# Performance work log

Measured on AMD Instinct MI355X. Metric: run time of the kernel, lower is better.

Reference implementation:

```python
import jax, jax.numpy as jnp
import numpy as np

N, E, M = 100000, 1600000, 10000
D_IN, D_HID, D_OUT = 128, 128, 128


def setup_inputs() -> dict:
    key = jax.random.key(0)
    ks = jax.random.split(key, 16)
    feat = jax.random.normal(ks[0], (N, D_IN), dtype=jnp.float32)
    src = jax.random.randint(ks[1], (E,), 0, N, dtype=jnp.int32)
    dst = jax.random.randint(ks[2], (E,), 0, N, dtype=jnp.int32)
    masked_offset = jax.random.randint(ks[3], (M,), 0, N, dtype=jnp.int32)
    def xavier(k, shape):
        fan_in, fan_out = shape[0], shape[1]
        a = jnp.sqrt(6.0 / (fan_in + fan_out))
        return jax.random.uniform(k, shape, jnp.float32, -a, a)
    return {
        'feat': feat, 'src': src, 'dst': dst, 'masked_offset': masked_offset,
        # GraphConv layers (weight [in,out], bias [out])
        'W1': xavier(ks[4], (D_IN, D_HID)), 'b1': jnp.zeros((D_HID,), jnp.float32),
        'W2': xavier(ks[5], (D_HID, D_HID)), 'b2': jnp.zeros((D_HID,), jnp.float32),
        # fusion MLP
        'Wm1': xavier(ks[6], (D_HID + D_IN, D_HID)), 'bm1': jnp.zeros((D_HID,), jnp.float32),
        'Wm2': xavier(ks[7], (D_HID, D_HID)), 'bm2': jnp.zeros((D_HID,), jnp.float32),
        'Wm3': xavier(ks[8], (D_HID, D_OUT)),  # final Linear has bias=False
    }


def _graph_conv_right(h, src, dst, W, b, inv_deg):
    # DGL GraphConv(norm='right'): aggregate src features at dst, divide by in-degree.
    # Apply weight first (in_feats >= out_feats path) -- mathematically identical.
    hw = h @ W                                   # [N, out]
    agg = jax.ops.segment_sum(hw[src], dst, num_segments=N)  # scatter-add over edges
    return agg * inv_deg + b


def reference(feat, src, dst, masked_offset, W1, b1, W2, b2, Wm1, bm1, Wm2, bm2, Wm3):
    ones = jnp.ones((E,), jnp.float32)
    deg = jax.ops.segment_sum(ones, dst, num_segments=N)
    inv_deg = (1.0 / jnp.clip(deg, 1.0, None))[:, None]      # [N,1]
    # GCN layer 1 + ReLU (Identity norm)
    h = jax.nn.relu(_graph_conv_right(feat, src, dst, W1, b1, inv_deg))
    # GCN layer 2 (last layer: no activation; dropout no-op at eval)
    h = _graph_conv_right(h, src, dst, W2, b2, inv_deg)
    # fusion == 'cat': relu(Identity(h[masked])) concat raw features
    hm = jax.nn.relu(h[masked_offset])                       # [M, H]
    x = jnp.concatenate([hm, feat[masked_offset]], axis=1)   # [M, H+D]
    x = jax.nn.relu(x @ Wm1 + bm1)
    x = jax.nn.relu(x @ Wm2 + bm2)
    return x @ Wm3
```

## Files before the change

kernel.cpp:

```cpp
#include <hip/hip_runtime.h>

#define NN 100000
#define NE 1600000
#define NM 10000
#define NSB 256
#define SUBN 391
#define CAP2 7424
#define PCH 2048

typedef __attribute__((ext_vector_type(8))) short bf16x8;
typedef __attribute__((ext_vector_type(4))) float f32x4;

__device__ inline float4 ld4(const float* p) { return *(const float4*)p; }
__device__ inline float bf2f(unsigned short u) {
  union { unsigned int i; float f; } c; c.i = ((unsigned int)u) << 16; return c.f;
}
__device__ inline unsigned short f2bf(float f) {
  union { float f; unsigned int i; } c; c.f = f;
  unsigned int u = c.i + 0x7fffu + ((c.i >> 16) & 1u);
  return (unsigned short)(u >> 16);
}
__device__ inline void stx(unsigned char* base, int rowBytes, int row, int col,
                           unsigned short val) {
  int bc = col * 2;
  int c = bc >> 4, cp = c ^ (row & 15);
  *(unsigned short*)&base[row * rowBytes + (cp << 4) + (bc & 15)] = val;
}
__device__ inline bf16x8 ldx8(const unsigned char* base, int rowBytes, int row, int kc) {
  return *(const bf16x8*)&base[row * rowBytes + ((kc ^ (row & 15)) << 4)];
}

__global__ __launch_bounds__(256) void part2_k(const int* __restrict__ src,
                                               const int* __restrict__ dst,
                                               unsigned* __restrict__ parts2,
                                               int* __restrict__ pcnt2) {
  __shared__ int cntw[4][NSB];
  __shared__ int basew[4][NSB];
  __shared__ int bstart[NSB + 1];
  __shared__ int gbase[NSB];
  __shared__ int wsum[4];
  __shared__ unsigned buf[PCH];
  __shared__ unsigned char bb[PCH];
  const int tid = threadIdx.x;
  const int wv = tid >> 6;
  const int e0 = blockIdx.x * PCH;

  for (int i = tid; i < 4 * NSB; i += 256) ((int*)cntw)[i] = 0;
  __syncthreads();

  unsigned pk[8];
  int b_[8], lp_[8];
#pragma unroll
  for (int j = 0; j < 8; ++j) {
    int e = e0 + j * 256 + tid;
    bool ok = e < NE;
    int s = ok ? src[e] : 0;
    int d = ok ? dst[e] : 0;
    int b = d / SUBN;
    int ld = d - b * SUBN;
    pk[j] = ((unsigned)ld << 17) | (unsigned)s;
    b_[j] = ok ? b : -1;
    if (ok) lp_[j] = atomicAdd(&cntw[wv][b], 1);
  }
  __syncthreads();
  int t0 = cntw[0][tid], t1 = cntw[1][tid], t2 = cntw[2][tid], t3 = cntw[3][tid];
  int tot = t0 + t1 + t2 + t3;
  int x = tot;
#pragma unroll
  for (int d = 1; d < 64; d <<= 1) {
    int y = __shfl_up(x, d, 64);
    if ((tid & 63) >= d) x += y;
  }
  if ((tid & 63) == 63) wsum[wv] = x;
  __syncthreads();
  int woff = 0;
#pragma unroll
  for (int w = 0; w < 4; ++w) woff += (w < wv) ? wsum[w] : 0;
  int excl = x + woff - tot;
  bstart[tid] = excl;
  basew[0][tid] = excl;
  basew[1][tid] = excl + t0;
  basew[2][tid] = excl + t0 + t1;
  basew[3][tid] = excl + t0 + t1 + t2;
  gbase[tid] = atomicAdd(&pcnt2[tid], tot);
  if (tid == NSB - 1) bstart[NSB] = excl + tot;
  __syncthreads();
#pragma unroll
  for (int j = 0; j < 8; ++j)
    if (b_[j] >= 0) {
      int pos = basew[wv][b_[j]] + lp_[j];
      buf[pos] = pk[j];
      bb[pos] = (unsigned char)b_[j];
    }
  __syncthreads();
  int total = bstart[NSB];
  for (int i = tid; i < total; i += 256) {
    int b = bb[i];
    int gi = gbase[b] + (i - bstart[b]);
    if (gi < CAP2) parts2[(size_t)b * CAP2 + gi] = buf[i];
  }
}

__global__ __launch_bounds__(1024) void deg2_k(const unsigned* __restrict__ parts2,
                                               const int* __restrict__ pcnt2,
                                               int* __restrict__ deg) {
  __shared__ int cnt[SUBN];
  int sb = blockIdx.x;
  int n = min(pcnt2[sb], CAP2);
  const unsigned* p = parts2 + (size_t)sb * CAP2;
  for (int i = threadIdx.x; i < SUBN; i += 1024) cnt[i] = 0;
  __syncthreads();
  for (int i = threadIdx.x; i < n; i += 1024) atomicAdd(&cnt[p[i] >> 17], 1);
  __syncthreads();
  int base = sb * SUBN;
  for (int i = threadIdx.x; i < SUBN; i += 1024)
    if (base + i < NN) deg[base + i] = cnt[i];
}

__global__ __launch_bounds__(1024) void scan1_k(const int* __restrict__ deg,
                                                int* __restrict__ excl,
                                                int* __restrict__ bsum, int n) {
  __shared__ int lds[1024];
  int tid = threadIdx.x;
  int gid = blockIdx.x * 1024 + tid;
  int v = (gid < n) ? deg[gid] : 0;
  lds[tid] = v;
  __syncthreads();
  for (int off = 1; off < 1024; off <<= 1) {
    int t = (tid >= off) ? lds[tid - off] : 0;
    __syncthreads();
    lds[tid] += t;
    __syncthreads();
  }
  if (gid < n) excl[gid] = lds[tid] - v;
  if (tid == 1023) bsum[blockIdx.x] = lds[1023];
}

__global__ void scan2_k(int* __restrict__ bsum, int nb) {
  __shared__ int lds[128];
  int tid = threadIdx.x;
  int v = (tid < nb) ? bsum[tid] : 0;
  lds[tid] = v;
  __syncthreads();
  for (int off = 1; off < 128; off <<= 1) {
    int t = (tid >= off) ? lds[tid - off] : 0;
    __syncthreads();
    lds[tid] += t;
    __syncthreads();
  }
  if (tid < nb) bsum[tid] = lds[tid] - v;
}

__global__ __launch_bounds__(256) void scan3_k(int* __restrict__ excl,
                                               const int* __restrict__ bsum,
                                               const int* __restrict__ deg,
                                               float* __restrict__ inv, int n) {
  int gid = blockIdx.x * 256 + threadIdx.x;
  if (gid < n) {
    excl[gid] += bsum[gid >> 10] + deg[gid];
    inv[gid] = 1.0f / fmaxf((float)deg[gid], 1.0f);
  }
}

__global__ __launch_bounds__(1024) void sort_emit_k(const unsigned* __restrict__ parts2,
                                                    const int* __restrict__ pcnt2,
                                                    const int* __restrict__ offs_end,
                                                    const int* __restrict__ degv,
                                                    int* __restrict__ csr) {
  __shared__ int cur[SUBN];
  __shared__ int sorted[CAP2];
  int sb = blockIdx.x;
  int n = min(pcnt2[sb], CAP2);
  const unsigned* p = parts2 + (size_t)sb * CAP2;
  int base = sb * SUBN;
  int segbase = offs_end[base] - degv[base];
  for (int i = threadIdx.x; i < SUBN; i += 1024) {
    int nd = base + i;
    cur[i] = (nd < NN) ? (offs_end[nd] - degv[nd]) : 0;
  }
  __syncthreads();
  for (int i = threadIdx.x; i < n; i += 1024) {
    unsigned v = p[i];
    int pos = atomicAdd(&cur[v >> 17], 1);
    sorted[pos - segbase] = (int)(v & 0x1FFFFu);
  }
  __syncthreads();
  for (int i = threadIdx.x; i < n; i += 1024) csr[segbase + i] = sorted[i];
}

__global__ __launch_bounds__(256) void tobf_k(const float* __restrict__ x,
                                              unsigned short* __restrict__ y, int n) {
  int idx = (blockIdx.x * 256 + threadIdx.x) * 4;
  if (idx < n) {
    float4 v = ld4(x + idx);
    unsigned int lo = (unsigned int)f2bf(v.x) | ((unsigned int)f2bf(v.y) << 16);
    unsigned int hi = (unsigned int)f2bf(v.z) | ((unsigned int)f2bf(v.w) << 16);
    *(uint2*)(y + idx) = make_uint2(lo, hi);
  }
}

__device__ inline void convfrag(const float* W, unsigned short* Wf, int g) {
  int k8 = (g >> 7) << 3, col = g & 127;
  unsigned short tmp[8];
#pragma unroll
  for (int i = 0; i < 8; ++i) tmp[i] = f2bf(W[(k8 + i) * 128 + col]);
  *(uint4*)&Wf[(size_t)g * 8] = *(const uint4*)tmp;
}
__global__ __launch_bounds__(256) void wconv_k(const float* W1, const float* W2,
                                               const float* Wm1, const float* Wm2,
                                               const float* Wm3,
                                               unsigned short* W1f, unsigned short* W2f,
                                               unsigned short* Wm1f, unsigned short* Wm2f,
                                               unsigned short* Wm3f) {
  int g = blockIdx.x * 256 + threadIdx.x;
  if (g < 2048) convfrag(W1, W1f, g);
  else if (g < 4096) convfrag(W2, W2f, g - 2048);
  else if (g < 8192) convfrag(Wm1, Wm1f, g - 4096);
  else if (g < 10240) convfrag(Wm2, Wm2f, g - 8192);
  else if (g < 12288) convfrag(Wm3, Wm3f, g - 10240);
}

__global__ __launch_bounds__(256) void mark_k(const int* __restrict__ masked,
                                              const int* __restrict__ csr,
                                              const int* __restrict__ offs_end,
                                              const int* __restrict__ degv,
                                              unsigned char* __restrict__ needed) {
  int m = blockIdx.x * 8 + (threadIdx.x >> 5);
  if (m >= NM) return;
  int lane = threadIdx.x & 31;
  int v = masked[m];
  int cnt = degv[v];
  int start = offs_end[v] - cnt;
  for (int i = lane; i < cnt; i += 32) needed[csr[start + i]] = 1;
}

__global__ __launch_bounds__(256) void fused_l1_k(const unsigned short* __restrict__ featbf,
                                                  const int* __restrict__ csr,
                                                  const int* __restrict__ offs_end,
                                                  const int* __restrict__ degv,
                                                  const float* __restrict__ inv,
                                                  const unsigned char* __restrict__ needed,
                                                  const unsigned short* __restrict__ W1f,
                                                  const float* __restrict__ b1,
                                                  unsigned short* __restrict__ h1bf) {
  __shared__ unsigned char lds[64 * 256];
  const int tid = threadIdx.x;
  const int rbase = blockIdx.x * 64;
  {
    int grp = tid >> 5, lane = tid & 31;
    const uint2* fb = (const uint2*)featbf;
    int c = lane >> 1;
    for (int k = 0; k < 8; ++k) {
      int row = grp * 8 + k;
      int v = rbase + row;
      unsigned char* dstp = &lds[row * 256 + (((c ^ (row & 15)) << 4)) + (lane & 1) * 8];
      if (v >= NN || !needed[v]) { *(uint2*)dstp = make_uint2(0u, 0u); continue; }
      int cnt = degv[v];
      int start = offs_end[v] - cnt;
      float a0 = 0.f, a1 = 0.f, a2 = 0.f, a3 = 0.f;
      int nb8 = (cnt + 7) >> 3;
      for (int it = 0; it < nb8; ++it) {
        int b = start + (it << 3);
        int rem = cnt - (it << 3);
        int sidx[8]; float msk[8];
#pragma unroll
        for (int j = 0; j < 8; ++j) {
          bool ok = j < rem;
          sidx[j] = csr[b + (ok ? j : 0)];
          msk[j] = ok ? 1.f : 0.f;
        }
        uint2 x[8];
#pragma unroll
        for (int j = 0; j < 8; ++j) x[j] = fb[(size_t)sidx[j] * 32 + lane];
#pragma unroll
        for (int j = 0; j < 8; ++j) {
          a0 = fmaf(msk[j], bf2f((unsigned short)(x[j].x)), a0);
          a1 = fmaf(msk[j], bf2f((unsigned short)(x[j].x >> 16)), a1);
          a2 = fmaf(msk[j], bf2f((unsigned short)(x[j].y)), a2);
          a3 = fmaf(msk[j], bf2f((unsigned short)(x[j].y >> 16)), a3);
        }
      }
      float iv = inv[v];
      unsigned int lo = (unsigned int)f2bf(a0 * iv) | ((unsigned int)f2bf(a1 * iv) << 16);
      unsigned int hi = (unsigned int)f2bf(a2 * iv) | ((unsigned int)f2bf(a3 * iv) << 16);
      *(uint2*)dstp = make_uint2(lo, hi);
    }
  }
  __syncthreads();
  const int wave = tid >> 6, lane = tid & 63, l15 = lane & 15, l4 = lane >> 4;
  int col0 = wave * 16 + l15, col1 = (wave + 4) * 16 + l15;
  float bias0 = b1[col0], bias1 = b1[col1];
  for (int rsub = 0; rsub < 4; ++rsub) {
    int row = rsub * 16 + l15;
    f32x4 acc0 = {0.f, 0.f, 0.f, 0.f};
    f32x4 acc1 = {0.f, 0.f, 0.f, 0.f};
#pragma unroll
    for (int kt = 0; kt < 4; ++kt) {
      int kc = kt * 4 + l4;
      bf16x8 a = ldx8(lds, 256, row, kc);
      bf16x8 b0 = *(const bf16x8*)&W1f[((size_t)kc * 128 + col0) * 8];
      bf16x8 b1v = *(const bf16x8*)&W1f[((size_t)kc * 128 + col1) * 8];
      acc0 = __builtin_amdgcn_mfma_f32_16x16x32_bf16(a, b0, acc0, 0, 0, 0);
      acc1 = __builtin_amdgcn_mfma_f32_16x16x32_bf16(a, b1v, acc1, 0, 0, 0);
    }
#pragma unroll
    for (int r = 0; r < 4; ++r) {
      int orow = rbase + rsub * 16 + l4 * 4 + r;
      if (orow < NN) {
        h1bf[(size_t)orow * 128 + col0] = f2bf(fmaxf(acc0[r] + bias0, 0.f));
        h1bf[(size_t)orow * 128 + col1] = f2bf(fmaxf(acc1[r] + bias1, 0.f));
      }
    }
  }
}

__global__ __launch_bounds__(256) void gather2_k(const unsigned short* __restrict__ h1bf,
                                                 const int* __restrict__ masked,
                                                 const int* __restrict__ csr,
                                                 const int* __restrict__ offs_end,
                                                 const int* __restrict__ degv,
                                                 const float* __restrict__ inv,
                                                 unsigned short* __restrict__ agg2bf) {
  int m = blockIdx.x * 8 + (threadIdx.x >> 5);
  if (m >= NM) return;
  int lane = threadIdx.x & 31;
  int v = masked[m];
  int cnt = degv[v];
  int start = offs_end[v] - cnt;
  const uint2* fb = (const uint2*)h1bf;
  float a0 = 0.f, a1 = 0.f, a2 = 0.f, a3 = 0.f;
  int nb8 = (cnt + 7) >> 3;
  for (int it = 0; it < nb8; ++it) {
    int b = start + (it << 3);
    int rem = cnt - (it << 3);
    int sidx[8]; float msk[8];
#pragma unroll
    for (int j = 0; j < 8; ++j) {
      bool ok = j < rem;
      sidx[j] = csr[b + (ok ? j : 0)];
      msk[j] = ok ? 1.f : 0.f;
    }
    uint2 x[8];
#pragma unroll
    for (int j = 0; j < 8; ++j) x[j] = fb[(size_t)sidx[j] * 32 + lane];
#pragma unroll
    for (int j = 0; j < 8; ++j) {
      a0 = fmaf(msk[j], bf2f((unsigned short)(x[j].x)), a0);
      a1 = fmaf(msk[j], bf2f((unsigned short)(x[j].x >> 16)), a1);
      a2 = fmaf(msk[j], bf2f((unsigned short)(x[j].y)), a2);
      a3 = fmaf(msk[j], bf2f((unsigned short)(x[j].y >> 16)), a3);
    }
  }
  float iv = inv[v];
  unsigned int lo = (unsigned int)f2bf(a0 * iv) | ((unsigned int)f2bf(a1 * iv) << 16);
  unsigned int hi = (unsigned int)f2bf(a2 * iv) | ((unsigned int)f2bf(a3 * iv) << 16);
  ((uint2*)agg2bf)[(size_t)m * 32 + lane] = make_uint2(lo, hi);
}

__global__ __launch_bounds__(256) void mlp_fused_k(const unsigned short* __restrict__ agg2bf,
                                                   const unsigned short* __restrict__ featbf,
                                                   const int* __restrict__ masked,
                                                   const unsigned short* __restrict__ W2f,
                                                   const float* __restrict__ b2,
                                                   const unsigned short* __restrict__ Wm1f,
                                                   const float* __restrict__ bm1,
                                                   const unsigned short* __restrict__ Wm2f,
                                                   const float* __restrict__ bm2,
                                                   const unsigned short* __restrict__ Wm3f,
                                                   float* __restrict__ out) {
  __shared__ unsigned char ldsX[64 * 512];
  __shared__ unsigned char ldsY[64 * 256];
  const int tid = threadIdx.x;
  const int rbase = blockIdx.x * 64;
  const int wave = tid >> 6, lane = tid & 63, l15 = lane & 15, l4 = lane >> 4;
  {
    int grp = tid >> 5, ln = tid & 31;
    uint2 vals[8];
#pragma unroll
    for (int k = 0; k < 8; ++k) {
      int m = rbase + grp * 8 + k;
      vals[k] = make_uint2(0u, 0u);
      if (m < NM) {
        int v = masked[m];
        vals[k] = ((const uint2*)featbf)[(size_t)v * 32 + ln];
      }
    }
#pragma unroll
    for (int k = 0; k < 8; ++k) {
      int row = grp * 8 + k;
      int c = 16 + (ln >> 1);
      *(uint2*)&ldsX[row * 512 + ((c ^ (row & 15)) << 4) + (ln & 1) * 8] = vals[k];
    }
  }
  {
    int col0 = wave * 16 + l15, col1 = (wave + 4) * 16 + l15;
    float bias0 = b2[col0], bias1 = b2[col1];
    for (int rsub = 0; rsub < 4; ++rsub) {
      int arow = rbase + rsub * 16 + l15;
      const unsigned short* ap = agg2bf + (size_t)min(arow, NM - 1) * 128;
      f32x4 acc0 = {0.f, 0.f, 0.f, 0.f};
      f32x4 acc1 = {0.f, 0.f, 0.f, 0.f};
#pragma unroll
      for (int kt = 0; kt < 4; ++kt) {
        int kc = kt * 4 + l4;
        bf16x8 a = *(const bf16x8*)(ap + kc * 8);
        bf16x8 b0 = *(const bf16x8*)&W2f[((size_t)kc * 128 + col0) * 8];
        bf16x8 b1v = *(const bf16x8*)&W2f[((size_t)kc * 128 + col1) * 8];
        acc0 = __builtin_amdgcn_mfma_f32_16x16x32_bf16(a, b0, acc0, 0, 0, 0);
        acc1 = __builtin_amdgcn_mfma_f32_16x16x32_bf16(a, b1v, acc1, 0, 0, 0);
      }
#pragma unroll
      for (int r = 0; r < 4; ++r) {
        int row = rsub * 16 + l4 * 4 + r;
        stx(ldsX, 512, row, col0, f2bf(fmaxf(acc0[r] + bias0, 0.f)));
        stx(ldsX, 512, row, col1, f2bf(fmaxf(acc1[r] + bias1, 0.f)));
      }
    }
  }
  __syncthreads();
  {
    int col0 = wave * 16 + l15, col1 = (wave + 4) * 16 + l15;
    float bias0 = bm1[col0], bias1 = bm1[col1];
    for (int rsub = 0; rsub < 4; ++rsub) {
      int row = rsub * 16 + l15;
      f32x4 acc0 = {0.f, 0.f, 0.f, 0.f};
      f32x4 acc1 = {0.f, 0.f, 0.f, 0.f};
#pragma unroll
      for (int kt = 0; kt < 8; ++kt) {
        int kc = kt * 4 + l4;
        bf16x8 a = ldx8(ldsX, 512, row, kc);
        bf16x8 b0 = *(const bf16x8*)&Wm1f[((size_t)kc * 128 + col0) * 8];
        bf16x8 b1v = *(const bf16x8*)&Wm1f[((size_t)kc * 128 + col1) * 8];
        acc0 = __builtin_amdgcn_mfma_f32_16x16x32_bf16(a, b0, acc0, 0, 0, 0);
        acc1 = __builtin_amdgcn_mfma_f32_16x16x32_bf16(a, b1v, acc1, 0, 0, 0);
      }
#pragma unroll
      for (int r = 0; r < 4; ++r) {
        int row2 = rsub * 16 + l4 * 4 + r;
        stx(ldsY, 256, row2, col0, f2bf(fmaxf(acc0[r] + bias0, 0.f)));
        stx(ldsY, 256, row2, col1, f2bf(fmaxf(acc1[r] + bias1, 0.f)));
      }
    }
  }
  __syncthreads();
  {
    int col0 = wave * 16 + l15, col1 = (wave + 4) * 16 + l15;
    float bias0 = bm2[col0], bias1 = bm2[col1];
    for (int rsub = 0; rsub < 4; ++rsub) {
      int row = rsub * 16 + l15;
      f32x4 acc0 = {0.f, 0.f, 0.f, 0.f};
      f32x4 acc1 = {0.f, 0.f, 0.f, 0.f};
#pragma unroll
      for (int kt = 0; kt < 4; ++kt) {
        int kc = kt * 4 + l4;
        bf16x8 a = ldx8(ldsY, 256, row, kc);
        bf16x8 b0 = *(const bf16x8*)&Wm2f[((size_t)kc * 128 + col0) * 8];
        bf16x8 b1v = *(const bf16x8*)&Wm2f[((size_t)kc * 128 + col1) * 8];
        acc0 = __builtin_amdgcn_mfma_f32_16x16x32_bf16(a, b0, acc0, 0, 0, 0);
        acc1 = __builtin_amdgcn_mfma_f32_16x16x32_bf16(a, b1v, acc1, 0, 0, 0);
      }
#pragma unroll
      for (int r = 0; r < 4; ++r) {
        int row2 = rsub * 16 + l4 * 4 + r;
        stx(ldsX, 256, row2, col0, f2bf(fmaxf(acc0[r] + bias0, 0.f)));
        stx(ldsX, 256, row2, col1, f2bf(fmaxf(acc1[r] + bias1, 0.f)));
      }
    }
  }
  __syncthreads();
  {
    int col0 = wave * 16 + l15, col1 = (wave + 4) * 16 + l15;
    for (int rsub = 0; rsub < 4; ++rsub) {
      int row = rsub * 16 + l15;
      f32x4 acc0 = {0.f, 0.f, 0.f, 0.f};
      f32x4 acc1 = {0.f, 0.f, 0.f, 0.f};
#pragma unroll
      for (int kt = 0; kt < 4; ++kt) {
        int kc = kt * 4 + l4;
        bf16x8 a = ldx8(ldsX, 256, row, kc);
        bf16x8 b0 = *(const bf16x8*)&Wm3f[((size_t)kc * 128 + col0) * 8];
        bf16x8 b1v = *(const bf16x8*)&Wm3f[((size_t)kc * 128 + col1) * 8];
        acc0 = __builtin_amdgcn_mfma_f32_16x16x32_bf16(a, b0, acc0, 0, 0, 0);
        acc1 = __builtin_amdgcn_mfma_f32_16x16x32_bf16(a, b1v, acc1, 0, 0, 0);
      }
#pragma unroll
      for (int r = 0; r < 4; ++r) {
        int orow = rbase + rsub * 16 + l4 * 4 + r;
        if (orow < NM) {
          out[(size_t)orow * 128 + col0] = acc0[r];
          out[(size_t)orow * 128 + col1] = acc1[r];
        }
      }
    }
  }
}

extern "C" void kernel_launch(void* const* d_in, const int* in_sizes, int n_in,
                              void* d_out, int out_size, void* d_ws, size_t ws_size,
                              hipStream_t stream) {
  const float* feat = (const float*)d_in[0];
  const int* src = (const int*)d_in[1];
  const int* dst = (const int*)d_in[2];
  const int* masked = (const int*)d_in[3];
  const float* W1 = (const float*)d_in[4];
  const float* b1 = (const float*)d_in[5];
  const float* W2 = (const float*)d_in[6];
  const float* b2 = (const float*)d_in[7];
  const float* Wm1 = (const float*)d_in[8];
  const float* bm1 = (const float*)d_in[9];
  const float* Wm2 = (const float*)d_in[10];
  const float* bm2 = (const float*)d_in[11];
  const float* Wm3 = (const float*)d_in[12];
  float* out = (float*)d_out;

  char* p = (char*)d_ws;
  int* deg = (int*)p;              p += (size_t)NN * 4;
  int* offs = (int*)p;             p += (size_t)NN * 4;
  int* bsum = (int*)p;             p += 128 * 4;
  int* pcnt2 = (int*)p;            p += NSB * 4;
  float* inv = (float*)p;          p += (size_t)NN * 4;
  int* csr = (int*)p;              p += (size_t)NE * 4;
  unsigned char* needed = (unsigned char*)p; p += (size_t)NN;
  p = (char*)(((size_t)p + 15) & ~(size_t)15);
  unsigned* parts2 = (unsigned*)p; p += (size_t)NSB * CAP2 * 4;
  unsigned short* featbf = (unsigned short*)p;  p += (size_t)NN * 128 * 2;
  unsigned short* h1bf = (unsigned short*)p;    p += (size_t)NN * 128 * 2;
  unsigned short* agg2bf = (unsigned short*)p;  p += (size_t)NM * 128 * 2;
  unsigned short* W1f = (unsigned short*)p;     p += 16384 * 2;
  unsigned short* W2f = (unsigned short*)p;     p += 16384 * 2;
  unsigned short* Wm1f = (unsigned short*)p;    p += 32768 * 2;
  unsigned short* Wm2f = (unsigned short*)p;    p += 16384 * 2;
  unsigned short* Wm3f = (unsigned short*)p;    p += 16384 * 2;

  (void)hipMemsetAsync(pcnt2, 0, NSB * 4, stream);
  (void)hipMemsetAsync(needed, 0, NN, stream);

  part2_k<<<(NE + PCH - 1) / PCH, 256, 0, stream>>>(src, dst, parts2, pcnt2);
  deg2_k<<<NSB, 1024, 0, stream>>>(parts2, pcnt2, deg);
  int nb = (NN + 1023) / 1024;
  scan1_k<<<nb, 1024, 0, stream>>>(deg, offs, bsum, NN);
  scan2_k<<<1, 128, 0, stream>>>(bsum, nb);
  scan3_k<<<(NN + 255) / 256, 256, 0, stream>>>(offs, bsum, deg, inv, NN);
  sort_emit_k<<<NSB, 1024, 0, stream>>>(parts2, pcnt2, offs, deg, csr);

  tobf_k<<<(NN * 128 / 4 + 255) / 256, 256, 0, stream>>>(feat, featbf, NN * 128);
  wconv_k<<<48, 256, 0, stream>>>(W1, W2, Wm1, Wm2, Wm3, W1f, W2f, Wm1f, Wm2f, Wm3f);

  mark_k<<<(NM + 7) / 8, 256, 0, stream>>>(masked, csr, offs, deg, needed);

  fused_l1_k<<<(NN + 63) / 64, 256, 0, stream>>>(featbf, csr, offs, deg, inv, needed,
                                                 W1f, b1, h1bf);
  gather2_k<<<(NM + 7) / 8, 256, 0, stream>>>(h1bf, masked, csr, offs, deg, inv, agg2bf);

  mlp_fused_k<<<(NM + 63) / 64, 256, 0, stream>>>(agg2bf, featbf, masked,
                                                  W2f, b2, Wm1f, bm1, Wm2f, bm2, Wm3f, out);
}
```

Measured before the change: 175.1 us.

## Slice features into column chunks and split layer-1 gather from MFMA

Node features and hidden activations are stored as eight column slices of 16 bf16 values each, so one slice (about 3.2 MB) can stay cache-resident during random neighbour gathers. A new slice-parallel gather kernel, driven by per-node metadata records, replaces the fused layer-1 gather+MFMA kernel and the layer-2 gather kernel. Layer 1's MFMA now runs as a separate pass reading the aggregated slices from global memory. In exchange, the CSR index lists are read once per slice, and an extra NN×128 intermediate is written to and read back from memory.

```diff
diff --git a/kernel.cpp b/kernel.cpp
--- a/kernel.cpp
+++ b/kernel.cpp
@@ -188,15 +188,18 @@
   for (int i = threadIdx.x; i < n; i += 1024) csr[segbase + i] = sorted[i];
 }
 
-__global__ __launch_bounds__(256) void tobf_k(const float* __restrict__ x,
-                                              unsigned short* __restrict__ y, int n) {
-  int idx = (blockIdx.x * 256 + threadIdx.x) * 4;
-  if (idx < n) {
-    float4 v = ld4(x + idx);
-    unsigned int lo = (unsigned int)f2bf(v.x) | ((unsigned int)f2bf(v.y) << 16);
-    unsigned int hi = (unsigned int)f2bf(v.z) | ((unsigned int)f2bf(v.w) << 16);
-    *(uint2*)(y + idx) = make_uint2(lo, hi);
-  }
+__global__ __launch_bounds__(256) void tobfs_k(const float* __restrict__ feat,
+                                               unsigned short* __restrict__ featsl) {
+  int t = blockIdx.x * 256 + threadIdx.x;
+  int v = t >> 4, part = t & 15;
+  if (v >= NN) return;
+  float4 u = ld4(feat + (size_t)v * 128 + part * 8);
+  float4 w = ld4(feat + (size_t)v * 128 + part * 8 + 4);
+  unsigned short tmp[8];
+  tmp[0] = f2bf(u.x); tmp[1] = f2bf(u.y); tmp[2] = f2bf(u.z); tmp[3] = f2bf(u.w);
+  tmp[4] = f2bf(w.x); tmp[5] = f2bf(w.y); tmp[6] = f2bf(w.z); tmp[7] = f2bf(w.w);
+  size_t idx = (size_t)(part >> 1) * NN * 2 + (size_t)v * 2 + (part & 1);
+  ((uint4*)featsl)[idx] = *(const uint4*)tmp;
 }
 
 __device__ inline void convfrag(const float* W, unsigned short* Wf, int g) {
@@ -224,7 +227,9 @@
                                               const int* __restrict__ csr,
                                               const int* __restrict__ offs_end,
                                               const int* __restrict__ degv,
-                                              unsigned char* __restrict__ needed) {
+                                              const float* __restrict__ inv,
+                                              unsigned char* __restrict__ needed,
+                                              uint4* __restrict__ meta2) {
   int m = blockIdx.x * 8 + (threadIdx.x >> 5);
   if (m >= NM) return;
   int lane = threadIdx.x & 31;
@@ -232,72 +237,86 @@
   int cnt = degv[v];
   int start = offs_end[v] - cnt;
   for (int i = lane; i < cnt; i += 32) needed[csr[start + i]] = 1;
-}
-
-__global__ __launch_bounds__(256) void fused_l1_k(const unsigned short* __restrict__ featbf,
-                                                  const int* __restrict__ csr,
-                                                  const int* __restrict__ offs_end,
-                                                  const int* __restrict__ degv,
-                                                  const float* __restrict__ inv,
-                                                  const unsigned char* __restrict__ needed,
-                                                  const unsigned short* __restrict__ W1f,
-                                                  const float* __restrict__ b1,
-                                                  unsigned short* __restrict__ h1bf) {
-  __shared__ unsigned char lds[64 * 256];
+  if (lane == 0)
+    meta2[m] = make_uint4((unsigned)start, (unsigned)cnt,
+                          (unsigned)__float_as_int(inv[v]), (unsigned)v);
+}
+
+__global__ __launch_bounds__(256) void meta1_k(const int* __restrict__ offs_end,
+                                               const int* __restrict__ degv,
+                                               const float* __restrict__ inv,
+                                               const unsigned char* __restrict__ needed,
+                                               uint4* __restrict__ meta1) {
+  int gid = blockIdx.x * 256 + threadIdx.x;
+  if (gid < NN) {
+    int c = degv[gid];
+    int st = offs_end[gid] - c;
+    meta1[gid] = make_uint4((unsigned)st,
+                            needed[gid] ? (unsigned)c : 0xFFFFFFFFu,
+                            (unsigned)__float_as_int(inv[gid]), 0u);
+  }
+}
+
+__global__ __launch_bounds__(256) void gatherS_k(const unsigned* __restrict__ fsl,
+                                                 const int* __restrict__ csr,
+                                                 const uint4* __restrict__ meta,
+                                                 unsigned* __restrict__ outS,
+                                                 int nNodes) {
+  const int s = blockIdx.x & 7;
+  const int g = blockIdx.x >> 3;
+  const int wv = threadIdx.x >> 6, lane = threadIdx.x & 63;
+  const int e = lane >> 3, c = lane & 7;
+  const unsigned* fs = fsl + (size_t)s * NN * 8;
+  unsigned* os = outS + (size_t)s * nNodes * 8;
+  for (int i = 0; i < 16; ++i) {
+    int v = g * 64 + wv * 16 + i;
+    if (v >= nNodes) break;
+    uint4 mt = meta[v];
+    int cnt = (int)mt.y;
+    if (cnt < 0) continue;
+    int start = (int)mt.x;
+    float iv = __int_as_float((int)mt.z);
+    float a0 = 0.f, a1 = 0.f;
+    for (int it = 0; it < cnt; it += 16) {
+      int j0 = it + e, j1 = it + 8 + e;
+      bool ok0 = j0 < cnt, ok1 = j1 < cnt;
+      int i0 = csr[start + (ok0 ? j0 : 0)];
+      int i1 = csr[start + (ok1 ? j1 : 0)];
+      unsigned x0 = fs[(size_t)i0 * 8 + c];
+      unsigned x1 = fs[(size_t)i1 * 8 + c];
+      float m0 = ok0 ? 1.f : 0.f, m1 = ok1 ? 1.f : 0.f;
+      a0 = fmaf(m0, bf2f((unsigned short)x0), a0);
+      a1 = fmaf(m0, bf2f((unsigned short)(x0 >> 16)), a1);
+      a0 = fmaf(m1, bf2f((unsigned short)x1), a0);
+      a1 = fmaf(m1, bf2f((unsigned short)(x1 >> 16)), a1);
+    }
+    a0 += __shfl_xor(a0, 8); a0 += __shfl_xor(a0, 16); a0 += __shfl_xor(a0, 32);
+    a1 += __shfl_xor(a1, 8); a1 += __shfl_xor(a1, 16); a1 += __shfl_xor(a1, 32);
+    if (e == 0) {
+      unsigned r = (unsigned)f2bf(a0 * iv) | ((unsigned)f2bf(a1 * iv) << 16);
+      os[(size_t)v * 8 + c] = r;
+    }
+  }
+}
+
+__global__ __launch_bounds__(256) void mfma1_k(const unsigned short* __restrict__ aggS,
+                                               const unsigned short* __restrict__ W1f,
+                                               const float* __restrict__ b1,
+                                               unsigned short* __restrict__ h1S) {
   const int tid = threadIdx.x;
+  const int wave = tid >> 6, lane = tid & 63, l15 = lane & 15, l4 = lane >> 4;
   const int rbase = blockIdx.x * 64;
-  {
-    int grp = tid >> 5, lane = tid & 31;
-    const uint2* fb = (const uint2*)featbf;
-    int c = lane >> 1;
-    for (int k = 0; k < 8; ++k) {
-      int row = grp * 8 + k;
-      int v = rbase + row;
-      unsigned char* dstp = &lds[row * 256 + (((c ^ (row & 15)) << 4)) + (lane & 1) * 8];
-      if (v >= NN || !needed[v]) { *(uint2*)dstp = make_uint2(0u, 0u); continue; }
-      int cnt = degv[v];
-      int start = offs_end[v] - cnt;
-      float a0 = 0.f, a1 = 0.f, a2 = 0.f, a3 = 0.f;
-      int nb8 = (cnt + 7) >> 3;
-      for (int it = 0; it < nb8; ++it) {
-        int b = start + (it << 3);
-        int rem = cnt - (it << 3);
-        int sidx[8]; float msk[8];
-#pragma unroll
-        for (int j = 0; j < 8; ++j) {
-          bool ok = j < rem;
-          sidx[j] = csr[b + (ok ? j : 0)];
-          msk[j] = ok ? 1.f : 0.f;
-        }
-        uint2 x[8];
-#pragma unroll
-        for (int j = 0; j < 8; ++j) x[j] = fb[(size_t)sidx[j] * 32 + lane];
-#pragma unroll
-        for (int j = 0; j < 8; ++j) {
-          a0 = fmaf(msk[j], bf2f((unsigned short)(x[j].x)), a0);
-          a1 = fmaf(msk[j], bf2f((unsigned short)(x[j].x >> 16)), a1);
-          a2 = fmaf(msk[j], bf2f((unsigned short)(x[j].y)), a2);
-          a3 = fmaf(msk[j], bf2f((unsigned short)(x[j].y >> 16)), a3);
-        }
-      }
-      float iv = inv[v];
-      unsigned int lo = (unsigned int)f2bf(a0 * iv) | ((unsigned int)f2bf(a1 * iv) << 16);
-      unsigned int hi = (unsigned int)f2bf(a2 * iv) | ((unsigned int)f2bf(a3 * iv) << 16);
-      *(uint2*)dstp = make_uint2(lo, hi);
-    }
-  }
-  __syncthreads();
-  const int wave = tid >> 6, lane = tid & 63, l15 = lane & 15, l4 = lane >> 4;
   int col0 = wave * 16 + l15, col1 = (wave + 4) * 16 + l15;
   float bias0 = b1[col0], bias1 = b1[col1];
   for (int rsub = 0; rsub < 4; ++rsub) {
-    int row = rsub * 16 + l15;
+    int arow = rbase + rsub * 16 + l15;
+    int ar = min(arow, NN - 1);
     f32x4 acc0 = {0.f, 0.f, 0.f, 0.f};
     f32x4 acc1 = {0.f, 0.f, 0.f, 0.f};
 #pragma unroll
     for (int kt = 0; kt < 4; ++kt) {
       int kc = kt * 4 + l4;
-      bf16x8 a = ldx8(lds, 256, row, kc);
+      bf16x8 a = *(const bf16x8*)&aggS[(size_t)(kc >> 1) * NN * 16 + (size_t)ar * 16 + (kc & 1) * 8];
       bf16x8 b0 = *(const bf16x8*)&W1f[((size_t)kc * 128 + col0) * 8];
       bf16x8 b1v = *(const bf16x8*)&W1f[((size_t)kc * 128 + col1) * 8];
       acc0 = __builtin_amdgcn_mfma_f32_16x16x32_bf16(a, b0, acc0, 0, 0, 0);
@@ -307,58 +326,15 @@
     for (int r = 0; r < 4; ++r) {
       int orow = rbase + rsub * 16 + l4 * 4 + r;
       if (orow < NN) {
-        h1bf[(size_t)orow * 128 + col0] = f2bf(fmaxf(acc0[r] + bias0, 0.f));
-        h1bf[(size_t)orow * 128 + col1] = f2bf(fmaxf(acc1[r] + bias1, 0.f));
-      }
-    }
-  }
-}
-
-__global__ __launch_bounds__(256) void gather2_k(const unsigned short* __restrict__ h1bf,
-                                                 const int* __restrict__ masked,
-                                                 const int* __restrict__ csr,
-                                                 const int* __restrict__ offs_end,
-                                                 const int* __restrict__ degv,
-                                                 const float* __restrict__ inv,
-                                                 unsigned short* __restrict__ agg2bf) {
-  int m = blockIdx.x * 8 + (threadIdx.x >> 5);
-  if (m >= NM) return;
-  int lane = threadIdx.x & 31;
-  int v = masked[m];
-  int cnt = degv[v];
-  int start = offs_end[v] - cnt;
-  const uint2* fb = (const uint2*)h1bf;
-  float a0 = 0.f, a1 = 0.f, a2 = 0.f, a3 = 0.f;
-  int nb8 = (cnt + 7) >> 3;
-  for (int it = 0; it < nb8; ++it) {
-    int b = start + (it << 3);
-    int rem = cnt - (it << 3);
-    int sidx[8]; float msk[8];
-#pragma unroll
-    for (int j = 0; j < 8; ++j) {
-      bool ok = j < rem;
-      sidx[j] = csr[b + (ok ? j : 0)];
-      msk[j] = ok ? 1.f : 0.f;
-    }
-    uint2 x[8];
-#pragma unroll
-    for (int j = 0; j < 8; ++j) x[j] = fb[(size_t)sidx[j] * 32 + lane];
-#pragma unroll
-    for (int j = 0; j < 8; ++j) {
-      a0 = fmaf(msk[j], bf2f((unsigned short)(x[j].x)), a0);
-      a1 = fmaf(msk[j], bf2f((unsigned short)(x[j].x >> 16)), a1);
-      a2 = fmaf(msk[j], bf2f((unsigned short)(x[j].y)), a2);
-      a3 = fmaf(msk[j], bf2f((unsigned short)(x[j].y >> 16)), a3);
-    }
-  }
-  float iv = inv[v];
-  unsigned int lo = (unsigned int)f2bf(a0 * iv) | ((unsigned int)f2bf(a1 * iv) << 16);
-  unsigned int hi = (unsigned int)f2bf(a2 * iv) | ((unsigned int)f2bf(a3 * iv) << 16);
-  ((uint2*)agg2bf)[(size_t)m * 32 + lane] = make_uint2(lo, hi);
-}
-
-__global__ __launch_bounds__(256) void mlp_fused_k(const unsigned short* __restrict__ agg2bf,
-                                                   const unsigned short* __restrict__ featbf,
+        h1S[(size_t)wave * NN * 16 + (size_t)orow * 16 + l15] = f2bf(fmaxf(acc0[r] + bias0, 0.f));
+        h1S[(size_t)(wave + 4) * NN * 16 + (size_t)orow * 16 + l15] = f2bf(fmaxf(acc1[r] + bias1, 0.f));
+      }
+    }
+  }
+}
+
+__global__ __launch_bounds__(256) void mlp_fused_k(const unsigned short* __restrict__ agg2S,
+                                                   const unsigned short* __restrict__ featsl,
                                                    const int* __restrict__ masked,
                                                    const unsigned short* __restrict__ W2f,
                                                    const float* __restrict__ b2,
@@ -382,7 +358,7 @@
       vals[k] = make_uint2(0u, 0u);
       if (m < NM) {
         int v = masked[m];
-        vals[k] = ((const uint2*)featbf)[(size_t)v * 32 + ln];
+        vals[k] = ((const uint2*)featsl)[(size_t)(ln >> 2) * NN * 4 + (size_t)v * 4 + (ln & 3)];
       }
     }
 #pragma unroll
@@ -397,13 +373,13 @@
     float bias0 = b2[col0], bias1 = b2[col1];
     for (int rsub = 0; rsub < 4; ++rsub) {
       int arow = rbase + rsub * 16 + l15;
-      const unsigned short* ap = agg2bf + (size_t)min(arow, NM - 1) * 128;
+      int ar = min(arow, NM - 1);
       f32x4 acc0 = {0.f, 0.f, 0.f, 0.f};
       f32x4 acc1 = {0.f, 0.f, 0.f, 0.f};
 #pragma unroll
       for (int kt = 0; kt < 4; ++kt) {
         int kc = kt * 4 + l4;
-        bf16x8 a = *(const bf16x8*)(ap + kc * 8);
+        bf16x8 a = *(const bf16x8*)&agg2S[(size_t)(kc >> 1) * NM * 16 + (size_t)ar * 16 + (kc & 1) * 8];
         bf16x8 b0 = *(const bf16x8*)&W2f[((size_t)kc * 128 + col0) * 8];
         bf16x8 b1v = *(const bf16x8*)&W2f[((size_t)kc * 128 + col1) * 8];
         acc0 = __builtin_amdgcn_mfma_f32_16x16x32_bf16(a, b0, acc0, 0, 0, 0);
@@ -522,10 +498,13 @@
   int* csr = (int*)p;              p += (size_t)NE * 4;
   unsigned char* needed = (unsigned char*)p; p += (size_t)NN;
   p = (char*)(((size_t)p + 15) & ~(size_t)15);
+  uint4* meta1 = (uint4*)p;        p += (size_t)NN * 16;
+  uint4* meta2 = (uint4*)p;        p += (size_t)NM * 16;
   unsigned* parts2 = (unsigned*)p; p += (size_t)NSB * CAP2 * 4;
-  unsigned short* featbf = (unsigned short*)p;  p += (size_t)NN * 128 * 2;
-  unsigned short* h1bf = (unsigned short*)p;    p += (size_t)NN * 128 * 2;
-  unsigned short* agg2bf = (unsigned short*)p;  p += (size_t)NM * 128 * 2;
+  unsigned short* featsl = (unsigned short*)p;  p += (size_t)NN * 128 * 2;
+  unsigned short* agg1S = (unsigned short*)p;   p += (size_t)NN * 128 * 2;
+  unsigned short* h1S = (unsigned short*)p;     p += (size_t)NN * 128 * 2;
+  unsigned short* agg2S = (unsigned short*)p;   p += (size_t)NM * 128 * 2;
   unsigned short* W1f = (unsigned short*)p;     p += 16384 * 2;
   unsigned short* W2f = (unsigned short*)p;     p += 16384 * 2;
   unsigned short* Wm1f = (unsigned short*)p;    p += 32768 * 2;
@@ -543,15 +522,19 @@
   scan3_k<<<(NN + 255) / 256, 256, 0, stream>>>(offs, bsum, deg, inv, NN);
   sort_emit_k<<<NSB, 1024, 0, stream>>>(parts2, pcnt2, offs, deg, csr);
 
-  tobf_k<<<(NN * 128 / 4 + 255) / 256, 256, 0, stream>>>(feat, featbf, NN * 128);
+  tobfs_k<<<(NN * 16 + 255) / 256, 256, 0, stream>>>(feat, featsl);
   wconv_k<<<48, 256, 0, stream>>>(W1, W2, Wm1, Wm2, Wm3, W1f, W2f, Wm1f, Wm2f, Wm3f);
 
-  mark_k<<<(NM + 7) / 8, 256, 0, stream>>>(masked, csr, offs, deg, needed);
-
-  fused_l1_k<<<(NN + 63) / 64, 256, 0, stream>>>(featbf, csr, offs, deg, inv, needed,
-                                                 W1f, b1, h1bf);
-  gather2_k<<<(NM + 7) / 8, 256, 0, stream>>>(h1bf, masked, csr, offs, deg, inv, agg2bf);
-
-  mlp_fused_k<<<(NM + 63) / 64, 256, 0, stream>>>(agg2bf, featbf, masked,
-                                                  W2f, b2, Wm1f, bm1, Wm2f, bm2, Wm3f, out);
-}
+  mark_k<<<(NM + 7) / 8, 256, 0, stream>>>(masked, csr, offs, deg, inv, needed, meta2);
+  meta1_k<<<(NN + 255) / 256, 256, 0, stream>>>(offs, deg, inv, needed, meta1);
+
+  gatherS_k<<<8 * 1563, 256, 0, stream>>>((const unsigned*)featsl, csr, meta1,
+                                          (unsigned*)agg1S, NN);
+  mfma1_k<<<1563, 256, 0, stream>>>(agg1S, W1f, b1, h1S);
+
+  gatherS_k<<<8 * 157, 256, 0, stream>>>((const unsigned*)h1S, csr, meta2,
+                                         (unsigned*)agg2S, NM);
+
+  mlp_fused_k<<<157, 256, 0, stream>>>(agg2S, featsl, masked,
+                                       W2f, b2, Wm1f, bm1, Wm2f, bm2, Wm3f, out);
+}
```

Measured after the change: 288.2 us. 64.6% more time.

## Split fused layer-1 gather+MFMA into per-node gather and separate GEMM kernel

Applied to the files above, without the earlier changes.

Replaces the fused layer-1 kernel with two kernels. In the old kernel each 32-lane group gathered 8 rows one after another, then did the MFMA matmul from LDS. Now a gather kernel assigns one 32-lane group per node, which raises memory-level parallelism for the latency-bound neighbour gather. A separate MFMA kernel reads the aggregated rows from global memory and keeps the W1 fragments in registers. The per-edge mask multiply is replaced by redirecting out-of-range slots to a zeroed sentinel row appended to the feature and h1 buffers, in both gathers. The cost is an extra global round-trip for the aggregated buffer and one more kernel launch. Rows that are not needed are left uninitialised in agg1, but they only feed h1 rows that are never read.

```diff
diff --git a/kernel.cpp b/kernel.cpp
--- a/kernel.cpp
+++ b/kernel.cpp
@@ -234,74 +234,75 @@
   for (int i = lane; i < cnt; i += 32) needed[csr[start + i]] = 1;
 }
 
-__global__ __launch_bounds__(256) void fused_l1_k(const unsigned short* __restrict__ featbf,
-                                                  const int* __restrict__ csr,
-                                                  const int* __restrict__ offs_end,
-                                                  const int* __restrict__ degv,
-                                                  const float* __restrict__ inv,
-                                                  const unsigned char* __restrict__ needed,
-                                                  const unsigned short* __restrict__ W1f,
-                                                  const float* __restrict__ b1,
-                                                  unsigned short* __restrict__ h1bf) {
-  __shared__ unsigned char lds[64 * 256];
+__global__ __launch_bounds__(256) void gather1_k(const unsigned short* __restrict__ featbf,
+                                                 const int* __restrict__ csr,
+                                                 const int* __restrict__ offs_end,
+                                                 const int* __restrict__ degv,
+                                                 const float* __restrict__ inv,
+                                                 const unsigned char* __restrict__ needed,
+                                                 unsigned short* __restrict__ agg1) {
+  int v = blockIdx.x * 8 + (threadIdx.x >> 5);
+  if (v >= NN) return;
+  if (!needed[v]) return;
+  int lane = threadIdx.x & 31;
+  int cnt = degv[v];
+  int start = offs_end[v] - cnt;
+  const uint2* fb = (const uint2*)featbf;
+  float a0 = 0.f, a1 = 0.f, a2 = 0.f, a3 = 0.f;
+  int nb8 = (cnt + 7) >> 3;
+  for (int it = 0; it < nb8; ++it) {
+    int b = start + (it << 3);
+    int rem = cnt - (it << 3);
+    int sidx[8];
+#pragma unroll
+    for (int j = 0; j < 8; ++j) {
+      int s = csr[b + (j < rem ? j : 0)];
+      sidx[j] = (j < rem) ? s : NN;
+    }
+    uint2 x[8];
+#pragma unroll
+    for (int j = 0; j < 8; ++j) x[j] = fb[(size_t)sidx[j] * 32 + lane];
+#pragma unroll
+    for (int j = 0; j < 8; ++j) {
+      a0 += bf2f((unsigned short)(x[j].x));
+      a1 += bf2f((unsigned short)(x[j].x >> 16));
+      a2 += bf2f((unsigned short)(x[j].y));
+      a3 += bf2f((unsigned short)(x[j].y >> 16));
+    }
+  }
+  float iv = inv[v];
+  unsigned int lo = (unsigned int)f2bf(a0 * iv) | ((unsigned int)f2bf(a1 * iv) << 16);
+  unsigned int hi = (unsigned int)f2bf(a2 * iv) | ((unsigned int)f2bf(a3 * iv) << 16);
+  ((uint2*)agg1)[(size_t)v * 32 + lane] = make_uint2(lo, hi);
+}
+
+__global__ __launch_bounds__(256) void mfma1_k(const unsigned short* __restrict__ agg1,
+                                               const unsigned short* __restrict__ W1f,
+                                               const float* __restrict__ b1,
+                                               unsigned short* __restrict__ h1bf) {
   const int tid = threadIdx.x;
+  const int wave = tid >> 6, lane = tid & 63, l15 = lane & 15, l4 = lane >> 4;
   const int rbase = blockIdx.x * 64;
-  {
-    int grp = tid >> 5, lane = tid & 31;
-    const uint2* fb = (const uint2*)featbf;
-    int c = lane >> 1;
-    for (int k = 0; k < 8; ++k) {
-      int row = grp * 8 + k;
-      int v = rbase + row;
-      unsigned char* dstp = &lds[row * 256 + (((c ^ (row & 15)) << 4)) + (lane & 1) * 8];
-      if (v >= NN || !needed[v]) { *(uint2*)dstp = make_uint2(0u, 0u); continue; }
-      int cnt = degv[v];
-      int start = offs_end[v] - cnt;
-      float a0 = 0.f, a1 = 0.f, a2 = 0.f, a3 = 0.f;
-      int nb8 = (cnt + 7) >> 3;
-      for (int it = 0; it < nb8; ++it) {
-        int b = start + (it << 3);
-        int rem = cnt - (it << 3);
-        int sidx[8]; float msk[8];
-#pragma unroll
-        for (int j = 0; j < 8; ++j) {
-          bool ok = j < rem;
-          sidx[j] = csr[b + (ok ? j : 0)];
-          msk[j] = ok ? 1.f : 0.f;
-        }
-        uint2 x[8];
-#pragma unroll
-        for (int j = 0; j < 8; ++j) x[j] = fb[(size_t)sidx[j] * 32 + lane];
-#pragma unroll
-        for (int j = 0; j < 8; ++j) {
-          a0 = fmaf(msk[j], bf2f((unsigned short)(x[j].x)), a0);
-          a1 = fmaf(msk[j], bf2f((unsigned short)(x[j].x >> 16)), a1);
-          a2 = fmaf(msk[j], bf2f((unsigned short)(x[j].y)), a2);
-          a3 = fmaf(msk[j], bf2f((unsigned short)(x[j].y >> 16)), a3);
-        }
-      }
-      float iv = inv[v];
-      unsigned int lo = (unsigned int)f2bf(a0 * iv) | ((unsigned int)f2bf(a1 * iv) << 16);
-      unsigned int hi = (unsigned int)f2bf(a2 * iv) | ((unsigned int)f2bf(a3 * iv) << 16);
-      *(uint2*)dstp = make_uint2(lo, hi);
-    }
-  }
-  __syncthreads();
-  const int wave = tid >> 6, lane = tid & 63, l15 = lane & 15, l4 = lane >> 4;
   int col0 = wave * 16 + l15, col1 = (wave + 4) * 16 + l15;
+  bf16x8 Bfr0[4], Bfr1[4];
+#pragma unroll
+  for (int kt = 0; kt < 4; ++kt) {
+    int kc = kt * 4 + l4;
+    Bfr0[kt] = *(const bf16x8*)&W1f[((size_t)kc * 128 + col0) * 8];
+    Bfr1[kt] = *(const bf16x8*)&W1f[((size_t)kc * 128 + col1) * 8];
+  }
   float bias0 = b1[col0], bias1 = b1[col1];
   for (int rsub = 0; rsub < 4; ++rsub) {
-    int row = rsub * 16 + l15;
+    int arow = rbase + rsub * 16 + l15;
+    const unsigned short* ap = agg1 + (size_t)min(arow, NN - 1) * 128;
     f32x4 acc0 = {0.f, 0.f, 0.f, 0.f};
     f32x4 acc1 = {0.f, 0.f, 0.f, 0.f};
 #pragma unroll
     for (int kt = 0; kt < 4; ++kt) {
       int kc = kt * 4 + l4;
-      bf16x8 a = ldx8(lds, 256, row, kc);
-      bf16x8 b0 = *(const bf16x8*)&W1f[((size_t)kc * 128 + col0) * 8];
-      bf16x8 b1v = *(const bf16x8*)&W1f[((size_t)kc * 128 + col1) * 8];
-      acc0 = __builtin_amdgcn_mfma_f32_16x16x32_bf16(a, b0, acc0, 0, 0, 0);
-      acc1 = __builtin_amdgcn_mfma_f32_16x16x32_bf16(a, b1v, acc1, 0, 0, 0);
+      bf16x8 a = *(const bf16x8*)(ap + kc * 8);
+      acc0 = __builtin_amdgcn_mfma_f32_16x16x32_bf16(a, Bfr0[kt], acc0, 0, 0, 0);
+      acc1 = __builtin_amdgcn_mfma_f32_16x16x32_bf16(a, Bfr1[kt], acc1, 0, 0, 0);
     }
 #pragma unroll
     for (int r = 0; r < 4; ++r) {
@@ -333,22 +334,21 @@
   for (int it = 0; it < nb8; ++it) {
     int b = start + (it << 3);
     int rem = cnt - (it << 3);
-    int sidx[8]; float msk[8];
+    int sidx[8];
 #pragma unroll
     for (int j = 0; j < 8; ++j) {
-      bool ok = j < rem;
-      sidx[j] = csr[b + (ok ? j : 0)];
-      msk[j] = ok ? 1.f : 0.f;
+      int s = csr[b + (j < rem ? j : 0)];
+      sidx[j] = (j < rem) ? s : NN;
     }
     uint2 x[8];
 #pragma unroll
     for (int j = 0; j < 8; ++j) x[j] = fb[(size_t)sidx[j] * 32 + lane];
 #pragma unroll
     for (int j = 0; j < 8; ++j) {
-      a0 = fmaf(msk[j], bf2f((unsigned short)(x[j].x)), a0);
-      a1 = fmaf(msk[j], bf2f((unsigned short)(x[j].x >> 16)), a1);
-      a2 = fmaf(msk[j], bf2f((unsigned short)(x[j].y)), a2);
-      a3 = fmaf(msk[j], bf2f((unsigned short)(x[j].y >> 16)), a3);
+      a0 += bf2f((unsigned short)(x[j].x));
+      a1 += bf2f((unsigned short)(x[j].x >> 16));
+      a2 += bf2f((unsigned short)(x[j].y));
+      a3 += bf2f((unsigned short)(x[j].y >> 16));
     }
   }
   float iv = inv[v];
@@ -523,8 +523,9 @@
   unsigned char* needed = (unsigned char*)p; p += (size_t)NN;
   p = (char*)(((size_t)p + 15) & ~(size_t)15);
   unsigned* parts2 = (unsigned*)p; p += (size_t)NSB * CAP2 * 4;
-  unsigned short* featbf = (unsigned short*)p;  p += (size_t)NN * 128 * 2;
-  unsigned short* h1bf = (unsigned short*)p;    p += (size_t)NN * 128 * 2;
+  unsigned short* featbf = (unsigned short*)p;  p += (size_t)(NN + 1) * 128 * 2;
+  unsigned short* agg1 = (unsigned short*)p;    p += (size_t)NN * 128 * 2;
+  unsigned short* h1bf = (unsigned short*)p;    p += (size_t)(NN + 1) * 128 * 2;
   unsigned short* agg2bf = (unsigned short*)p;  p += (size_t)NM * 128 * 2;
   unsigned short* W1f = (unsigned short*)p;     p += 16384 * 2;
   unsigned short* W2f = (unsigned short*)p;     p += 16384 * 2;
@@ -534,6 +535,8 @@
 
   (void)hipMemsetAsync(pcnt2, 0, NSB * 4, stream);
   (void)hipMemsetAsync(needed, 0, NN, stream);
+  (void)hipMemsetAsync(featbf + (size_t)NN * 128, 0, 256, stream);
+  (void)hipMemsetAsync(h1bf + (size_t)NN * 128, 0, 256, stream);
 
   part2_k<<<(NE + PCH - 1) / PCH, 256, 0, stream>>>(src, dst, parts2, pcnt2);
   deg2_k<<<NSB, 1024, 0, stream>>>(parts2, pcnt2, deg);
@@ -548,8 +551,9 @@
 
   mark_k<<<(NM + 7) / 8, 256, 0, stream>>>(masked, csr, offs, deg, needed);
 
-  fused_l1_k<<<(NN + 63) / 64, 256, 0, stream>>>(featbf, csr, offs, deg, inv, needed,
-                                                 W1f, b1, h1bf);
+  gather1_k<<<(NN + 7) / 8, 256, 0, stream>>>(featbf, csr, offs, deg, inv, needed, agg1);
+  mfma1_k<<<(NN + 63) / 64, 256, 0, stream>>>(agg1, W1f, b1, h1bf);
+
   gather2_k<<<(NM + 7) / 8, 256, 0, stream>>>(h1bf, masked, csr, offs, deg, inv, agg2bf);
 
   mlp_fused_k<<<(NM + 63) / 64, 256, 0, stream>>>(agg2bf, featbf, masked,
```

After: 185.1 us. 5.7% more time.
